# Performance work log

Hardware: AMD Instinct MI355X
Metric: run time of the kernel (lower is better)

## Reference

```python
import jax, jax.numpy as jnp
import numpy as np

B = 65536        # batch of (Z, N) token pairs
V = 512          # vocab size per input
D = 1024         # hidden_dim == embedding_dim
IN = 2 * D       # input_dim = embedding_dim * len(vocab_size)
E = 4            # num_experts (hardcoded in MoEModel)
OUT = 128        # output_dim


def setup_inputs() -> dict:
    key = jax.random.key(0)
    ks = jax.random.split(key, 6)
    x = jax.random.randint(ks[0], (B, 2), 0, V, dtype=jnp.int64)
    emb0 = jax.random.normal(ks[1], (V, D), dtype=jnp.float32)
    emb1 = jax.random.normal(ks[2], (V, D), dtype=jnp.float32)
    W1 = jax.random.normal(ks[3], (E, IN, D), dtype=jnp.float32) * 0.02
    b1 = jnp.zeros((E, D), dtype=jnp.float32)
    W2 = jax.random.normal(ks[4], (E, D, OUT), dtype=jnp.float32) * 0.02
    b2 = jnp.zeros((E, OUT), dtype=jnp.float32)
    Wg = jax.random.normal(ks[5], (IN, E), dtype=jnp.float32) * 0.02
    bg = jnp.zeros((E,), dtype=jnp.float32)
    return {"x": x, "emb0": emb0, "emb1": emb1, "W1": W1, "b1": b1,
            "W2": W2, "b2": b2, "Wg": Wg, "bg": bg}


def reference(x, emb0, emb1, W1, b1, W2, b2, Wg, bg):
    # embed_input: gather each column's embedding and concat -> [B, IN]
    e = jnp.concatenate([emb0[x[:, 0]], emb1[x[:, 1]]], axis=1)
    # gating network: softmax(MuReadout(e)) -> [B, E]
    gates = jax.nn.softmax(e @ Wg + bg, axis=-1)
    # all 4 experts run densely: Linear -> SiLU -> MuReadout, batched over E
    h = jax.nn.silu(jnp.einsum('bi,eid->bed', e, W1) + b1)      # [B, E, D]
    expert_out = jnp.einsum('bed,edo->beo', h, W2) + b2          # [B, E, OUT]
    # einsum('ij,ikj->ik') combine: softmax-weighted mixture over experts
    out = jnp.einsum('be,beo->bo', gates, expert_out)            # [B, OUT]
    return out
```

## Files before the change

kernel.cpp:

```cpp
#include <hip/hip_runtime.h>


typedef __attribute__((ext_vector_type(8))) short short8;
typedef __attribute__((ext_vector_type(4))) float f32x4;

static __device__ __forceinline__ unsigned short f2b(float f) {
  unsigned int u = __builtin_bit_cast(unsigned int, f);
  u += 0x7fffu + ((u >> 16) & 1u);
  return (unsigned short)(u >> 16);
}
static __device__ __forceinline__ float bflo(unsigned int u) {
  return __builtin_bit_cast(float, u << 16);
}
static __device__ __forceinline__ float bfhi(unsigned int u) {
  return __builtin_bit_cast(float, u & 0xffff0000u);
}

#define BARRIER() do { asm volatile("s_waitcnt lgkmcnt(0)" ::: "memory"); \
                       __builtin_amdgcn_s_barrier(); } while (0)

__global__ void prep_g(const float* __restrict__ emb0, const float* __restrict__ emb1,
                       const float* __restrict__ Wg, const float* __restrict__ bg,
                       float* __restrict__ G0, float* __restrict__ G1) {
  const int bid = blockIdx.x;
  const int half = bid >> 9;
  const int v = bid & 511;
  const float* __restrict__ emb = half ? emb1 : emb0;
  const float* __restrict__ wg = Wg + (size_t)half * 1024 * 4;
  float a0 = 0.f, a1 = 0.f, a2 = 0.f, a3 = 0.f;
  for (int i = threadIdx.x; i < 1024; i += 256) {
    const float ev = emb[(size_t)v * 1024 + i];
    const float4 w = *(const float4*)(wg + (size_t)i * 4);
    a0 += ev * w.x; a1 += ev * w.y; a2 += ev * w.z; a3 += ev * w.w;
  }
  __shared__ float red[4][256];
  red[0][threadIdx.x] = a0; red[1][threadIdx.x] = a1;
  red[2][threadIdx.x] = a2; red[3][threadIdx.x] = a3;
  __syncthreads();
  for (int s = 128; s > 0; s >>= 1) {
    if (threadIdx.x < s) {
      red[0][threadIdx.x] += red[0][threadIdx.x + s];
      red[1][threadIdx.x] += red[1][threadIdx.x + s];
      red[2][threadIdx.x] += red[2][threadIdx.x + s];
      red[3][threadIdx.x] += red[3][threadIdx.x + s];
    }
    __syncthreads();
  }
  if (threadIdx.x < 4) {
    const float val = red[threadIdx.x][0] + (half == 0 ? bg[threadIdx.x] : 0.f);
    (half ? G1 : G0)[(size_t)v * 4 + threadIdx.x] = val;
  }
}

__global__ void prep_w2(const float* __restrict__ W2, unsigned short* __restrict__ W2T) {
  __shared__ float st[64][65];
  const int kt = blockIdx.x, ot = blockIdx.y;
  const int tid = threadIdx.x;
  for (int it = 0; it < 16; ++it) {
    const int idx = it * 256 + tid;
    const int k = idx >> 6, o = idx & 63;
    st[k][o] = W2[(size_t)(kt * 64 + k) * 128 + ot * 64 + o];
  }
  __syncthreads();
  for (int it = 0; it < 4; ++it) {
    const int idx = it * 256 + tid;
    const int o = idx >> 4, c = idx & 15;
    const unsigned int p0 =
        (unsigned int)f2b(st[c * 4 + 0][o]) | ((unsigned int)f2b(st[c * 4 + 1][o]) << 16);
    const unsigned int p1 =
        (unsigned int)f2b(st[c * 4 + 2][o]) | ((unsigned int)f2b(st[c * 4 + 3][o]) << 16);
    *(uint2*)(W2T + (size_t)(ot * 64 + o) * 4096 + kt * 64 + c * 4) = make_uint2(p0, p1);
  }
}

__global__ void prep_emb(const float* __restrict__ emb0, const float* __restrict__ emb1,
                         unsigned short* __restrict__ E0, unsigned short* __restrict__ E1) {
  const float* __restrict__ src = blockIdx.y ? emb1 : emb0;
  unsigned short* __restrict__ dst = blockIdx.y ? E1 : E0;
  const size_t base = (size_t)blockIdx.x * 2048 + (size_t)threadIdx.x * 8;
  const float4 lo = *(const float4*)(src + base);
  const float4 hi = *(const float4*)(src + base + 4);
  short8 o;
  o[0] = (short)f2b(lo.x); o[1] = (short)f2b(lo.y);
  o[2] = (short)f2b(lo.z); o[3] = (short)f2b(lo.w);
  o[4] = (short)f2b(hi.x); o[5] = (short)f2b(hi.y);
  o[6] = (short)f2b(hi.z); o[7] = (short)f2b(hi.w);
  *(short8*)(dst + base) = o;
}

__global__ void prep_w1t(const float* __restrict__ W1, unsigned short* __restrict__ W1T) {
  __shared__ float st[64][65];
  const int z = blockIdx.y;
  const int kt = blockIdx.x >> 4, dt = blockIdx.x & 15;
  const int e = z >> 1, half = z & 1;
  const int tid = threadIdx.x;
  const int r = tid >> 2, cg = (tid & 3) * 16;
  const float* src = W1 + ((size_t)e * 2048 + half * 1024 + kt * 64 + r) * 1024 + dt * 64 + cg;
#pragma unroll
  for (int j = 0; j < 4; ++j) {
    const float4 v = *(const float4*)(src + j * 4);
    st[r][cg + j * 4 + 0] = v.x; st[r][cg + j * 4 + 1] = v.y;
    st[r][cg + j * 4 + 2] = v.z; st[r][cg + j * 4 + 3] = v.w;
  }
  __syncthreads();
  const int dr = tid >> 2, kb = (tid & 3) * 16;
  short8 o0, o1;
#pragma unroll
  for (int m = 0; m < 8; ++m) o0[m] = (short)f2b(st[kb + m][dr]);
#pragma unroll
  for (int m = 0; m < 8; ++m) o1[m] = (short)f2b(st[kb + 8 + m][dr]);
  unsigned short* dst = W1T + ((size_t)z * 1024 + dt * 64 + dr) * 1024 + kt * 64 + kb;
  *(short8*)dst = o0;
  *(short8*)(dst + 8) = o1;
}

__launch_bounds__(256, 2)
__global__ void build_tables(const unsigned short* __restrict__ E0,
                             const unsigned short* __restrict__ E1,
                             const unsigned short* __restrict__ W1T,
                             const float* __restrict__ b1,
                             unsigned short* __restrict__ T0, unsigned short* __restrict__ T1) {
  __shared__ unsigned short At[128 * 64];
  __shared__ unsigned short Bt[64 * 64];

  const int bid = blockIdx.x;
  const int z = bid >> 6, rem = bid & 63;
  const int vt = rem >> 4, dt = rem & 15;
  const int e = z >> 1, half = z & 1;
  const unsigned short* __restrict__ E = half ? E1 : E0;
  const unsigned short* __restrict__ Wp = W1T + (size_t)z * 1024 * 1024;
  unsigned short* __restrict__ Tout = (half ? T1 : T0) + (size_t)e * 512 * 1024;

  const int tid = threadIdx.x, lane = tid & 63, wave = tid >> 6;
  const int wm = wave >> 1, wn = wave & 1;

  const int arow = tid >> 1, ah = tid & 1;
  int wAoff[4];
#pragma unroll
  for (int i = 0; i < 4; ++i)
    wAoff[i] = arow * 128 + ((ah * 64 + i * 16) ^ ((arow & 7) << 4));
  const int bcol = tid >> 2, bc = tid & 3;
  int wBoff[2];
#pragma unroll
  for (int i = 0; i < 2; ++i)
    wBoff[i] = bcol * 128 + ((bc * 32 + i * 16) ^ ((bcol & 7) << 4));

  const unsigned short* aSrc = E + (size_t)(vt * 128 + arow) * 1024 + ah * 32;
  const unsigned short* bSrc = Wp + (size_t)(dt * 64 + bcol) * 1024 + bc * 16;

  const int kq = (lane >> 4) * 16;
  int rAoff[4], rAsw[4], rBoff[2], rBsw[2];
#pragma unroll
  for (int mi = 0; mi < 4; ++mi) {
    const int ra = wm * 64 + mi * 16 + (lane & 15);
    rAoff[mi] = ra * 128; rAsw[mi] = (ra & 7) << 4;
  }
#pragma unroll
  for (int ni = 0; ni < 2; ++ni) {
    const int cb = wn * 32 + ni * 16 + (lane & 15);
    rBoff[ni] = cb * 128; rBsw[ni] = (cb & 7) << 4;
  }

  f32x4 acc[4][2] = {};
  uint4 ea[4]; uint4 eb[2];

  auto issueLoads = [&](int kt2) {
    const int k0 = kt2 * 64;
#pragma unroll
    for (int i = 0; i < 4; ++i) ea[i] = *(const uint4*)(aSrc + k0 + i * 8);
#pragma unroll
    for (int i = 0; i < 2; ++i) eb[i] = *(const uint4*)(bSrc + k0 + i * 8);
  };

  issueLoads(0);
  for (int kt2 = 0; kt2 < 16; ++kt2) {
    BARRIER();
#pragma unroll
    for (int i = 0; i < 4; ++i) *(uint4*)((char*)At + wAoff[i]) = ea[i];
#pragma unroll
    for (int i = 0; i < 2; ++i) *(uint4*)((char*)Bt + wBoff[i]) = eb[i];
    if (kt2 < 15) issueLoads(kt2 + 1);
    BARRIER();
#pragma unroll
    for (int kk = 0; kk < 2; ++kk) {
      const int kb = kk * 64 + kq;
      short8 af[4], bfr[2];
#pragma unroll
      for (int mi = 0; mi < 4; ++mi)
        af[mi] = *(const short8*)((char*)At + rAoff[mi] + (kb ^ rAsw[mi]));
#pragma unroll
      for (int ni = 0; ni < 2; ++ni)
        bfr[ni] = *(const short8*)((char*)Bt + rBoff[ni] + (kb ^ rBsw[ni]));
#pragma unroll
      for (int mi = 0; mi < 4; ++mi)
#pragma unroll
        for (int ni = 0; ni < 2; ++ni)
          acc[mi][ni] = __builtin_amdgcn_mfma_f32_16x16x32_bf16(af[mi], bfr[ni], acc[mi][ni], 0, 0, 0);
    }
  }
  const float* bb = b1 + (size_t)e * 1024;
#pragma unroll
  for (int ni = 0; ni < 2; ++ni) {
    const int dcol = dt * 64 + wn * 32 + ni * 16 + (lane & 15);
    const float bias = (half == 0) ? bb[dcol] : 0.f;
#pragma unroll
    for (int mi = 0; mi < 4; ++mi) {
      const int vrow0 = vt * 128 + wm * 64 + mi * 16 + ((lane >> 4) << 2);
      const f32x4 a = acc[mi][ni];
#pragma unroll
      for (int j = 0; j < 4; ++j)
        Tout[(size_t)(vrow0 + j) * 1024 + dcol] = f2b(a[j] + bias);
    }
  }
}

__launch_bounds__(512, 4)
__global__ void moe_main(const int* __restrict__ X,
                         const unsigned short* __restrict__ T0,
                         const unsigned short* __restrict__ T1,
                         const unsigned short* __restrict__ W2T,
                         const float* __restrict__ G0,
                         const float* __restrict__ G1,
                         const float* __restrict__ b2v,
                         float* __restrict__ out) {
  __shared__ unsigned short At[128 * 64];
  __shared__ unsigned short Bt[128 * 64];
  __shared__ float gl[128 * 4];
  __shared__ int xs0[128], xs1[128];

  const int tid = threadIdx.x, lane = tid & 63, wave = tid >> 6;
  const int wm = wave >> 1, wn = wave & 1;
  int bid = blockIdx.x;
  bid = (bid & 7) * 64 + (bid >> 3);
  const int b0 = bid * 128;

  if (tid < 128) {
    const int b = b0 + tid;
    const int x0 = X[2 * b], x1 = X[2 * b + 1];
    xs0[tid] = x0; xs1[tid] = x1;
    const float4 l0 = *(const float4*)(G0 + 4 * x0);
    const float4 l1 = *(const float4*)(G1 + 4 * x1);
    const float z0 = l0.x + l1.x, z1 = l0.y + l1.y;
    const float z2 = l0.z + l1.z, z3 = l0.w + l1.w;
    const float m = fmaxf(fmaxf(z0, z1), fmaxf(z2, z3));
    const float e0 = __expf(z0 - m), e1 = __expf(z1 - m);
    const float e2 = __expf(z2 - m), e3 = __expf(z3 - m);
    const float inv = __builtin_amdgcn_rcpf(e0 + e1 + e2 + e3);
    *(float4*)(&gl[4 * tid]) = make_float4(e0 * inv, e1 * inv, e2 * inv, e3 * inv);
  }
  __syncthreads();

  const int arow = tid >> 2, ac = tid & 3;
  const int sx0 = xs0[arow], sx1 = xs1[arow];
  const float4 grow = *(const float4*)(&gl[4 * arow]);
  int wOff[2];
#pragma unroll
  for (int i = 0; i < 2; ++i)
    wOff[i] = arow * 128 + ((ac * 32 + i * 16) ^ ((arow & 7) << 4));

  const int kq = (lane >> 4) * 16;
  int rAoff[2], rAsw[2], rBoff[4], rBsw[4];
#pragma unroll
  for (int mi = 0; mi < 2; ++mi) {
    const int ra = wm * 32 + mi * 16 + (lane & 15);
    rAoff[mi] = ra * 128; rAsw[mi] = (ra & 7) << 4;
  }
#pragma unroll
  for (int ni = 0; ni < 4; ++ni) {
    const int cb = wn * 64 + ni * 16 + (lane & 15);
    rBoff[ni] = cb * 128; rBsw[ni] = (cb & 7) << 4;
  }

  f32x4 acc[2][4] = {};
  uint4 ua[2], ub[2], bw[2];

  auto issueLoads = [&](int t) {
    const int e = t >> 4, d0 = (t & 15) << 6;
    const unsigned short* p0 = T0 + (((size_t)(e * 512 + sx0)) << 10) + d0 + ac * 16;
    const unsigned short* p1 = T1 + (((size_t)(e * 512 + sx1)) << 10) + d0 + ac * 16;
    const unsigned short* pb = W2T + (size_t)arow * 4096 + t * 64 + ac * 16;
    ua[0] = *(const uint4*)p0; ua[1] = *(const uint4*)(p0 + 8);
    ub[0] = *(const uint4*)p1; ub[1] = *(const uint4*)(p1 + 8);
    bw[0] = *(const uint4*)pb; bw[1] = *(const uint4*)(pb + 8);
  };

  issueLoads(0);
  for (int t = 0; t < 64; ++t) {
    const int e = t >> 4;
    const float g = (e == 0) ? grow.x : (e == 1) ? grow.y : (e == 2) ? grow.z : grow.w;
    short8 sa[2];
#pragma unroll
    for (int i = 0; i < 2; ++i) {
      float f[8];
      f[0] = bflo(ua[i].x) + bflo(ub[i].x);
      f[1] = bfhi(ua[i].x) + bfhi(ub[i].x);
      f[2] = bflo(ua[i].y) + bflo(ub[i].y);
      f[3] = bfhi(ua[i].y) + bfhi(ub[i].y);
      f[4] = bflo(ua[i].z) + bflo(ub[i].z);
      f[5] = bfhi(ua[i].z) + bfhi(ub[i].z);
      f[6] = bflo(ua[i].w) + bflo(ub[i].w);
      f[7] = bfhi(ua[i].w) + bfhi(ub[i].w);
      short8 o8;
#pragma unroll
      for (int j = 0; j < 8; ++j) {
        const float tv = f[j];
        const float sg = g * tv * __builtin_amdgcn_rcpf(1.f + __expf(-tv));
        o8[j] = (short)f2b(sg);
      }
      sa[i] = o8;
    }
    BARRIER();
    *(uint4*)((char*)At + wOff[0]) = *(uint4*)&sa[0];
    *(uint4*)((char*)At + wOff[1]) = *(uint4*)&sa[1];
    *(uint4*)((char*)Bt + wOff[0]) = bw[0];
    *(uint4*)((char*)Bt + wOff[1]) = bw[1];
    if (t < 63) issueLoads(t + 1);
    BARRIER();
#pragma unroll
    for (int kk = 0; kk < 2; ++kk) {
      const int kb = kk * 64 + kq;
      short8 af[2], bfr[4];
#pragma unroll
      for (int mi = 0; mi < 2; ++mi)
        af[mi] = *(const short8*)((char*)At + rAoff[mi] + (kb ^ rAsw[mi]));
#pragma unroll
      for (int ni = 0; ni < 4; ++ni)
        bfr[ni] = *(const short8*)((char*)Bt + rBoff[ni] + (kb ^ rBsw[ni]));
#pragma unroll
      for (int mi = 0; mi < 2; ++mi)
#pragma unroll
        for (int ni = 0; ni < 4; ++ni)
          acc[mi][ni] = __builtin_amdgcn_mfma_f32_16x16x32_bf16(af[mi], bfr[ni], acc[mi][ni], 0, 0, 0);
    }
  }

#pragma unroll
  for (int ni = 0; ni < 4; ++ni) {
    const int col = wn * 64 + ni * 16 + (lane & 15);
    const float c0 = b2v[col], c1 = b2v[128 + col];
    const float c2 = b2v[256 + col], c3 = b2v[384 + col];
#pragma unroll
    for (int mi = 0; mi < 2; ++mi) {
      const int row0 = wm * 32 + mi * 16 + ((lane >> 4) << 2);
      const f32x4 a = acc[mi][ni];
#pragma unroll
      for (int j = 0; j < 4; ++j) {
        const int row = row0 + j;
        const float4 g = *(const float4*)(&gl[4 * row]);
        out[(size_t)(b0 + row) * 128 + col] = a[j] + g.x * c0 + g.y * c1 + g.z * c2 + g.w * c3;
      }
    }
  }
}

extern "C" void kernel_launch(void* const* d_in, const int* in_sizes, int n_in,
                              void* d_out, int out_size, void* d_ws, size_t ws_size,
                              hipStream_t stream) {
  const int*   X    = (const int*)  d_in[0];
  const float* emb0 = (const float*)d_in[1];
  const float* emb1 = (const float*)d_in[2];
  const float* W1   = (const float*)d_in[3];
  const float* b1   = (const float*)d_in[4];
  const float* W2   = (const float*)d_in[5];
  const float* b2   = (const float*)d_in[6];
  const float* Wg   = (const float*)d_in[7];
  const float* bg   = (const float*)d_in[8];
  float* out = (float*)d_out;

  char* ws = (char*)d_ws;
  const size_t MB = 1024 * 1024;
  unsigned short* T0  = (unsigned short*)(ws);
  unsigned short* T1  = (unsigned short*)(ws + 4 * MB);
  unsigned short* W2T = (unsigned short*)(ws + 8 * MB);
  float* G0 = (float*)(ws + 9 * MB);
  float* G1 = (float*)(ws + 9 * MB + 8192);
  unsigned short* E0  = (unsigned short*)(ws + 10 * MB);
  unsigned short* E1  = (unsigned short*)(ws + 11 * MB);
  unsigned short* W1T = (unsigned short*)(ws + 12 * MB);

  hipLaunchKernelGGL(prep_emb, dim3(256, 2), dim3(256), 0, stream, emb0, emb1, E0, E1);
  hipLaunchKernelGGL(prep_w1t, dim3(256, 8), dim3(256), 0, stream, W1, W1T);
  hipLaunchKernelGGL(prep_w2, dim3(64, 2), dim3(256), 0, stream, W2, W2T);
  hipLaunchKernelGGL(prep_g, dim3(1024), dim3(256), 0, stream, emb0, emb1, Wg, bg, G0, G1);
  hipLaunchKernelGGL(build_tables, dim3(512), dim3(256), 0, stream, E0, E1, W1T, b1, T0, T1);
  hipLaunchKernelGGL(moe_main, dim3(512), dim3(512), 0, stream, X, T0, T1, W2T, G0, G1, b2, out);
}
```

Baseline: 346.0 us.

## Fuse prep kernels, double-buffer register prefetch, and stage output stores through LDS

Merges the four preprocessing kernels into a single launch dispatched by block index, and switches bf16 packing to the hardware v_cvt_pk_bf16_f32 instruction. build_tables drops to 64x64 tiles with twice as many blocks and higher occupancy, double-buffers its register prefetch, and writes results through LDS so global stores are coalesced. moe_main double-buffers the gathered table loads, raises wave priority around the MFMA section, and stages the fp32 output through LDS for vectorized coalesced stores. These changes target launch overhead, load latency and scattered stores, at the cost of more registers and extra barriers.

Result: slower. 387.5 us (+12.0%).

```diff
diff --git a/kernel.cpp b/kernel.cpp
--- a/kernel.cpp
+++ b/kernel.cpp
@@ -15,116 +15,119 @@
 static __device__ __forceinline__ float bfhi(unsigned int u) {
   return __builtin_bit_cast(float, u & 0xffff0000u);
 }
+static __device__ __forceinline__ unsigned int cvtpk(float a, float b) {
+  unsigned int r;
+  asm("v_cvt_pk_bf16_f32 %0, %1, %2" : "=v"(r) : "v"(a), "v"(b));
+  return r;
+}
 
 #define BARRIER() do { asm volatile("s_waitcnt lgkmcnt(0)" ::: "memory"); \
                        __builtin_amdgcn_s_barrier(); } while (0)
 
-__global__ void prep_g(const float* __restrict__ emb0, const float* __restrict__ emb1,
-                       const float* __restrict__ Wg, const float* __restrict__ bg,
-                       float* __restrict__ G0, float* __restrict__ G1) {
+__global__ void prep_all(const float* __restrict__ emb0, const float* __restrict__ emb1,
+                         const float* __restrict__ Wg, const float* __restrict__ bg,
+                         const float* __restrict__ W2, const float* __restrict__ W1,
+                         float* __restrict__ G0, float* __restrict__ G1,
+                         unsigned short* __restrict__ E0, unsigned short* __restrict__ E1,
+                         unsigned short* __restrict__ W2T, unsigned short* __restrict__ W1T) {
+  __shared__ __align__(16) char sm[16640];
   const int bid = blockIdx.x;
-  const int half = bid >> 9;
-  const int v = bid & 511;
-  const float* __restrict__ emb = half ? emb1 : emb0;
-  const float* __restrict__ wg = Wg + (size_t)half * 1024 * 4;
-  float a0 = 0.f, a1 = 0.f, a2 = 0.f, a3 = 0.f;
-  for (int i = threadIdx.x; i < 1024; i += 256) {
-    const float ev = emb[(size_t)v * 1024 + i];
-    const float4 w = *(const float4*)(wg + (size_t)i * 4);
-    a0 += ev * w.x; a1 += ev * w.y; a2 += ev * w.z; a3 += ev * w.w;
-  }
-  __shared__ float red[4][256];
-  red[0][threadIdx.x] = a0; red[1][threadIdx.x] = a1;
-  red[2][threadIdx.x] = a2; red[3][threadIdx.x] = a3;
-  __syncthreads();
-  for (int s = 128; s > 0; s >>= 1) {
-    if (threadIdx.x < s) {
-      red[0][threadIdx.x] += red[0][threadIdx.x + s];
-      red[1][threadIdx.x] += red[1][threadIdx.x + s];
-      red[2][threadIdx.x] += red[2][threadIdx.x + s];
-      red[3][threadIdx.x] += red[3][threadIdx.x + s];
-    }
+  const int tid = threadIdx.x;
+  if (bid < 1024) {
+    float (*red)[256] = (float(*)[256])sm;
+    const int half = bid >> 9, v = bid & 511;
+    const float* __restrict__ emb = half ? emb1 : emb0;
+    const float* __restrict__ wg = Wg + (size_t)half * 1024 * 4;
+    float a0 = 0.f, a1 = 0.f, a2 = 0.f, a3 = 0.f;
+    for (int i = tid; i < 1024; i += 256) {
+      const float ev = emb[(size_t)v * 1024 + i];
+      const float4 w = *(const float4*)(wg + (size_t)i * 4);
+      a0 += ev * w.x; a1 += ev * w.y; a2 += ev * w.z; a3 += ev * w.w;
+    }
+    red[0][tid] = a0; red[1][tid] = a1; red[2][tid] = a2; red[3][tid] = a3;
     __syncthreads();
-  }
-  if (threadIdx.x < 4) {
-    const float val = red[threadIdx.x][0] + (half == 0 ? bg[threadIdx.x] : 0.f);
-    (half ? G1 : G0)[(size_t)v * 4 + threadIdx.x] = val;
-  }
-}
-
-__global__ void prep_w2(const float* __restrict__ W2, unsigned short* __restrict__ W2T) {
-  __shared__ float st[64][65];
-  const int kt = blockIdx.x, ot = blockIdx.y;
-  const int tid = threadIdx.x;
-  for (int it = 0; it < 16; ++it) {
-    const int idx = it * 256 + tid;
-    const int k = idx >> 6, o = idx & 63;
-    st[k][o] = W2[(size_t)(kt * 64 + k) * 128 + ot * 64 + o];
-  }
-  __syncthreads();
-  for (int it = 0; it < 4; ++it) {
-    const int idx = it * 256 + tid;
-    const int o = idx >> 4, c = idx & 15;
-    const unsigned int p0 =
-        (unsigned int)f2b(st[c * 4 + 0][o]) | ((unsigned int)f2b(st[c * 4 + 1][o]) << 16);
-    const unsigned int p1 =
-        (unsigned int)f2b(st[c * 4 + 2][o]) | ((unsigned int)f2b(st[c * 4 + 3][o]) << 16);
-    *(uint2*)(W2T + (size_t)(ot * 64 + o) * 4096 + kt * 64 + c * 4) = make_uint2(p0, p1);
-  }
-}
-
-__global__ void prep_emb(const float* __restrict__ emb0, const float* __restrict__ emb1,
-                         unsigned short* __restrict__ E0, unsigned short* __restrict__ E1) {
-  const float* __restrict__ src = blockIdx.y ? emb1 : emb0;
-  unsigned short* __restrict__ dst = blockIdx.y ? E1 : E0;
-  const size_t base = (size_t)blockIdx.x * 2048 + (size_t)threadIdx.x * 8;
-  const float4 lo = *(const float4*)(src + base);
-  const float4 hi = *(const float4*)(src + base + 4);
-  short8 o;
-  o[0] = (short)f2b(lo.x); o[1] = (short)f2b(lo.y);
-  o[2] = (short)f2b(lo.z); o[3] = (short)f2b(lo.w);
-  o[4] = (short)f2b(hi.x); o[5] = (short)f2b(hi.y);
-  o[6] = (short)f2b(hi.z); o[7] = (short)f2b(hi.w);
-  *(short8*)(dst + base) = o;
-}
-
-__global__ void prep_w1t(const float* __restrict__ W1, unsigned short* __restrict__ W1T) {
-  __shared__ float st[64][65];
-  const int z = blockIdx.y;
-  const int kt = blockIdx.x >> 4, dt = blockIdx.x & 15;
-  const int e = z >> 1, half = z & 1;
-  const int tid = threadIdx.x;
-  const int r = tid >> 2, cg = (tid & 3) * 16;
-  const float* src = W1 + ((size_t)e * 2048 + half * 1024 + kt * 64 + r) * 1024 + dt * 64 + cg;
-#pragma unroll
-  for (int j = 0; j < 4; ++j) {
-    const float4 v = *(const float4*)(src + j * 4);
-    st[r][cg + j * 4 + 0] = v.x; st[r][cg + j * 4 + 1] = v.y;
-    st[r][cg + j * 4 + 2] = v.z; st[r][cg + j * 4 + 3] = v.w;
-  }
-  __syncthreads();
-  const int dr = tid >> 2, kb = (tid & 3) * 16;
-  short8 o0, o1;
-#pragma unroll
-  for (int m = 0; m < 8; ++m) o0[m] = (short)f2b(st[kb + m][dr]);
-#pragma unroll
-  for (int m = 0; m < 8; ++m) o1[m] = (short)f2b(st[kb + 8 + m][dr]);
-  unsigned short* dst = W1T + ((size_t)z * 1024 + dt * 64 + dr) * 1024 + kt * 64 + kb;
-  *(short8*)dst = o0;
-  *(short8*)(dst + 8) = o1;
-}
-
-__launch_bounds__(256, 2)
+    for (int s = 128; s > 0; s >>= 1) {
+      if (tid < s) {
+        red[0][tid] += red[0][tid + s]; red[1][tid] += red[1][tid + s];
+        red[2][tid] += red[2][tid + s]; red[3][tid] += red[3][tid + s];
+      }
+      __syncthreads();
+    }
+    if (tid < 4) {
+      const float val = red[tid][0] + (half == 0 ? bg[tid] : 0.f);
+      (half ? G1 : G0)[(size_t)v * 4 + tid] = val;
+    }
+  } else if (bid < 1536) {
+    const int idx = bid - 1024;
+    const int half = idx >> 8, blk = idx & 255;
+    const float* __restrict__ src = half ? emb1 : emb0;
+    unsigned short* __restrict__ dst = half ? E1 : E0;
+    const size_t base = (size_t)blk * 2048 + (size_t)tid * 8;
+    const float4 lo = *(const float4*)(src + base);
+    const float4 hi = *(const float4*)(src + base + 4);
+    uint4 o;
+    o.x = cvtpk(lo.x, lo.y); o.y = cvtpk(lo.z, lo.w);
+    o.z = cvtpk(hi.x, hi.y); o.w = cvtpk(hi.z, hi.w);
+    *(uint4*)(dst + base) = o;
+  } else if (bid < 1664) {
+    float (*st)[65] = (float(*)[65])sm;
+    const int idx = bid - 1536;
+    const int kt = idx & 63, ot = idx >> 6;
+    for (int it = 0; it < 16; ++it) {
+      const int i2 = it * 256 + tid;
+      const int k = i2 >> 6, o = i2 & 63;
+      st[k][o] = W2[(size_t)(kt * 64 + k) * 128 + ot * 64 + o];
+    }
+    __syncthreads();
+    for (int it = 0; it < 4; ++it) {
+      const int i2 = it * 256 + tid;
+      const int o = i2 >> 4, c = i2 & 15;
+      const unsigned int p0 = cvtpk(st[c * 4 + 0][o], st[c * 4 + 1][o]);
+      const unsigned int p1 = cvtpk(st[c * 4 + 2][o], st[c * 4 + 3][o]);
+      *(uint2*)(W2T + (size_t)(ot * 64 + o) * 4096 + kt * 64 + c * 4) = make_uint2(p0, p1);
+    }
+  } else {
+    float (*st)[65] = (float(*)[65])sm;
+    const int idx = bid - 1664;
+    const int z = idx >> 8, xx = idx & 255;
+    const int kt = xx >> 4, dt = xx & 15;
+    const int e = z >> 1, half = z & 1;
+    const int r = tid >> 2, cg = (tid & 3) * 16;
+    const float* src = W1 + ((size_t)e * 2048 + half * 1024 + kt * 64 + r) * 1024 + dt * 64 + cg;
+#pragma unroll
+    for (int j = 0; j < 4; ++j) {
+      const float4 v = *(const float4*)(src + j * 4);
+      st[r][cg + j * 4 + 0] = v.x; st[r][cg + j * 4 + 1] = v.y;
+      st[r][cg + j * 4 + 2] = v.z; st[r][cg + j * 4 + 3] = v.w;
+    }
+    __syncthreads();
+    const int dr = tid >> 2, kb = (tid & 3) * 16;
+    uint4 o0, o1;
+    o0.x = cvtpk(st[kb + 0][dr], st[kb + 1][dr]);
+    o0.y = cvtpk(st[kb + 2][dr], st[kb + 3][dr]);
+    o0.z = cvtpk(st[kb + 4][dr], st[kb + 5][dr]);
+    o0.w = cvtpk(st[kb + 6][dr], st[kb + 7][dr]);
+    o1.x = cvtpk(st[kb + 8][dr], st[kb + 9][dr]);
+    o1.y = cvtpk(st[kb + 10][dr], st[kb + 11][dr]);
+    o1.z = cvtpk(st[kb + 12][dr], st[kb + 13][dr]);
+    o1.w = cvtpk(st[kb + 14][dr], st[kb + 15][dr]);
+    unsigned short* dst = W1T + ((size_t)z * 1024 + dt * 64 + dr) * 1024 + kt * 64 + kb;
+    *(uint4*)dst = o0;
+    *(uint4*)(dst + 8) = o1;
+  }
+}
+
+__launch_bounds__(256, 4)
 __global__ void build_tables(const unsigned short* __restrict__ E0,
                              const unsigned short* __restrict__ E1,
                              const unsigned short* __restrict__ W1T,
                              const float* __restrict__ b1,
                              unsigned short* __restrict__ T0, unsigned short* __restrict__ T1) {
-  __shared__ unsigned short At[128 * 64];
-  __shared__ unsigned short Bt[64 * 64];
+  __shared__ __align__(16) unsigned short At[64 * 64];
+  __shared__ __align__(16) unsigned short Bt[64 * 64];
 
   const int bid = blockIdx.x;
-  const int z = bid >> 6, rem = bid & 63;
+  const int z = bid >> 7, rem = bid & 127;
   const int vt = rem >> 4, dt = rem & 15;
   const int e = z >> 1, half = z & 1;
   const unsigned short* __restrict__ E = half ? E1 : E0;
@@ -134,83 +137,101 @@
   const int tid = threadIdx.x, lane = tid & 63, wave = tid >> 6;
   const int wm = wave >> 1, wn = wave & 1;
 
-  const int arow = tid >> 1, ah = tid & 1;
-  int wAoff[4];
-#pragma unroll
-  for (int i = 0; i < 4; ++i)
-    wAoff[i] = arow * 128 + ((ah * 64 + i * 16) ^ ((arow & 7) << 4));
-  const int bcol = tid >> 2, bc = tid & 3;
-  int wBoff[2];
+  const int arow = tid >> 2, ac = tid & 3;
+  int wOff[2];
 #pragma unroll
   for (int i = 0; i < 2; ++i)
-    wBoff[i] = bcol * 128 + ((bc * 32 + i * 16) ^ ((bcol & 7) << 4));
-
-  const unsigned short* aSrc = E + (size_t)(vt * 128 + arow) * 1024 + ah * 32;
-  const unsigned short* bSrc = Wp + (size_t)(dt * 64 + bcol) * 1024 + bc * 16;
+    wOff[i] = arow * 128 + ((ac * 32 + i * 16) ^ ((arow & 7) << 4));
+  const unsigned short* aSrc = E + (size_t)(vt * 64 + arow) * 1024 + ac * 16;
+  const unsigned short* bSrc = Wp + (size_t)(dt * 64 + arow) * 1024 + ac * 16;
 
   const int kq = (lane >> 4) * 16;
-  int rAoff[4], rAsw[4], rBoff[2], rBsw[2];
-#pragma unroll
-  for (int mi = 0; mi < 4; ++mi) {
-    const int ra = wm * 64 + mi * 16 + (lane & 15);
+  int rAoff[2], rAsw[2], rBoff[2], rBsw[2];
+#pragma unroll
+  for (int mi = 0; mi < 2; ++mi) {
+    const int ra = wm * 32 + mi * 16 + (lane & 15);
     rAoff[mi] = ra * 128; rAsw[mi] = (ra & 7) << 4;
-  }
-#pragma unroll
-  for (int ni = 0; ni < 2; ++ni) {
-    const int cb = wn * 32 + ni * 16 + (lane & 15);
-    rBoff[ni] = cb * 128; rBsw[ni] = (cb & 7) << 4;
-  }
-
-  f32x4 acc[4][2] = {};
-  uint4 ea[4]; uint4 eb[2];
-
-  auto issueLoads = [&](int kt2) {
-    const int k0 = kt2 * 64;
-#pragma unroll
-    for (int i = 0; i < 4; ++i) ea[i] = *(const uint4*)(aSrc + k0 + i * 8);
-#pragma unroll
-    for (int i = 0; i < 2; ++i) eb[i] = *(const uint4*)(bSrc + k0 + i * 8);
-  };
-
-  issueLoads(0);
-  for (int kt2 = 0; kt2 < 16; ++kt2) {
-    BARRIER();
-#pragma unroll
-    for (int i = 0; i < 4; ++i) *(uint4*)((char*)At + wAoff[i]) = ea[i];
-#pragma unroll
-    for (int i = 0; i < 2; ++i) *(uint4*)((char*)Bt + wBoff[i]) = eb[i];
-    if (kt2 < 15) issueLoads(kt2 + 1);
-    BARRIER();
+    const int cb = wn * 32 + mi * 16 + (lane & 15);
+    rBoff[mi] = cb * 128; rBsw[mi] = (cb & 7) << 4;
+  }
+
+  f32x4 acc[2][2] = {};
+  uint4 eaA[2], ebA[2], eaB[2], ebB[2];
+
+  auto issue = [&](int kt, uint4* ea, uint4* eb) {
+    const int k0 = kt * 64;
+    ea[0] = *(const uint4*)(aSrc + k0); ea[1] = *(const uint4*)(aSrc + k0 + 8);
+    eb[0] = *(const uint4*)(bSrc + k0); eb[1] = *(const uint4*)(bSrc + k0 + 8);
+  };
+  auto mfmaStep = [&]() {
 #pragma unroll
     for (int kk = 0; kk < 2; ++kk) {
       const int kb = kk * 64 + kq;
-      short8 af[4], bfr[2];
-#pragma unroll
-      for (int mi = 0; mi < 4; ++mi)
+      short8 af[2], bfr[2];
+#pragma unroll
+      for (int mi = 0; mi < 2; ++mi)
         af[mi] = *(const short8*)((char*)At + rAoff[mi] + (kb ^ rAsw[mi]));
 #pragma unroll
       for (int ni = 0; ni < 2; ++ni)
         bfr[ni] = *(const short8*)((char*)Bt + rBoff[ni] + (kb ^ rBsw[ni]));
 #pragma unroll
-      for (int mi = 0; mi < 4; ++mi)
+      for (int mi = 0; mi < 2; ++mi)
 #pragma unroll
         for (int ni = 0; ni < 2; ++ni)
           acc[mi][ni] = __builtin_amdgcn_mfma_f32_16x16x32_bf16(af[mi], bfr[ni], acc[mi][ni], 0, 0, 0);
     }
-  }
+  };
+
+  issue(0, eaA, ebA);
+  issue(1, eaB, ebB);
+  for (int kt = 0; kt < 16; kt += 2) {
+    BARRIER();
+#pragma unroll
+    for (int i = 0; i < 2; ++i) {
+      *(uint4*)((char*)At + wOff[i]) = eaA[i];
+      *(uint4*)((char*)Bt + wOff[i]) = ebA[i];
+    }
+    if (kt + 2 < 16) issue(kt + 2, eaA, ebA);
+    BARRIER();
+    __builtin_amdgcn_s_setprio(1);
+    mfmaStep();
+    __builtin_amdgcn_s_setprio(0);
+    BARRIER();
+#pragma unroll
+    for (int i = 0; i < 2; ++i) {
+      *(uint4*)((char*)At + wOff[i]) = eaB[i];
+      *(uint4*)((char*)Bt + wOff[i]) = ebB[i];
+    }
+    if (kt + 3 < 16) issue(kt + 3, eaB, ebB);
+    BARRIER();
+    __builtin_amdgcn_s_setprio(1);
+    mfmaStep();
+    __builtin_amdgcn_s_setprio(0);
+  }
+
   const float* bb = b1 + (size_t)e * 1024;
+  unsigned short* fs = At;
+  BARRIER();
 #pragma unroll
   for (int ni = 0; ni < 2; ++ni) {
-    const int dcol = dt * 64 + wn * 32 + ni * 16 + (lane & 15);
-    const float bias = (half == 0) ? bb[dcol] : 0.f;
-#pragma unroll
-    for (int mi = 0; mi < 4; ++mi) {
-      const int vrow0 = vt * 128 + wm * 64 + mi * 16 + ((lane >> 4) << 2);
+    const int lc = wn * 32 + ni * 16 + (lane & 15);
+    const float bias = (half == 0) ? bb[dt * 64 + lc] : 0.f;
+#pragma unroll
+    for (int mi = 0; mi < 2; ++mi) {
+      const int r0 = wm * 32 + mi * 16 + ((lane >> 4) << 2);
       const f32x4 a = acc[mi][ni];
 #pragma unroll
-      for (int j = 0; j < 4; ++j)
-        Tout[(size_t)(vrow0 + j) * 1024 + dcol] = f2b(a[j] + bias);
-    }
+      for (int j = 0; j < 4; ++j) fs[(r0 + j) * 64 + lc] = f2b(a[j] + bias);
+    }
+  }
+  BARRIER();
+  {
+    const int r = tid >> 2, c = (tid & 3) * 16;
+    const uint4 w0 = *(const uint4*)(fs + r * 64 + c);
+    const uint4 w1 = *(const uint4*)(fs + r * 64 + c + 8);
+    unsigned short* op = Tout + (size_t)(vt * 64 + r) * 1024 + dt * 64 + c;
+    *(uint4*)op = w0;
+    *(uint4*)(op + 8) = w1;
   }
 }
 
@@ -223,10 +244,12 @@
                          const float* __restrict__ G1,
                          const float* __restrict__ b2v,
                          float* __restrict__ out) {
-  __shared__ unsigned short At[128 * 64];
-  __shared__ unsigned short Bt[128 * 64];
-  __shared__ float gl[128 * 4];
-  __shared__ int xs0[128], xs1[128];
+  __shared__ __align__(16) char smem[35840];
+  unsigned short* At = (unsigned short*)smem;
+  unsigned short* Bt = (unsigned short*)(smem + 16384);
+  float* gl = (float*)(smem + 32768);
+  int* xs0 = (int*)(smem + 34816);
+  int* xs1 = (int*)(smem + 35328);
 
   const int tid = threadIdx.x, lane = tid & 63, wave = tid >> 6;
   const int wm = wave >> 1, wn = wave & 1;
@@ -272,50 +295,37 @@
   }
 
   f32x4 acc[2][4] = {};
-  uint4 ua[2], ub[2], bw[2];
-
-  auto issueLoads = [&](int t) {
+  uint4 uaA[2], ubA[2], uaB[2], ubB[2], bw[2];
+
+  auto issueA = [&](int t, uint4* ua, uint4* ub) {
     const int e = t >> 4, d0 = (t & 15) << 6;
     const unsigned short* p0 = T0 + (((size_t)(e * 512 + sx0)) << 10) + d0 + ac * 16;
     const unsigned short* p1 = T1 + (((size_t)(e * 512 + sx1)) << 10) + d0 + ac * 16;
-    const unsigned short* pb = W2T + (size_t)arow * 4096 + t * 64 + ac * 16;
     ua[0] = *(const uint4*)p0; ua[1] = *(const uint4*)(p0 + 8);
     ub[0] = *(const uint4*)p1; ub[1] = *(const uint4*)(p1 + 8);
+  };
+  auto issueB = [&](int t) {
+    const unsigned short* pb = W2T + (size_t)arow * 4096 + t * 64 + ac * 16;
     bw[0] = *(const uint4*)pb; bw[1] = *(const uint4*)(pb + 8);
   };
-
-  issueLoads(0);
-  for (int t = 0; t < 64; ++t) {
-    const int e = t >> 4;
-    const float g = (e == 0) ? grow.x : (e == 1) ? grow.y : (e == 2) ? grow.z : grow.w;
-    short8 sa[2];
+  auto siluPack = [&](const uint4* ua, const uint4* ub, float g, uint4* sw) {
 #pragma unroll
     for (int i = 0; i < 2; ++i) {
-      float f[8];
-      f[0] = bflo(ua[i].x) + bflo(ub[i].x);
-      f[1] = bfhi(ua[i].x) + bfhi(ub[i].x);
-      f[2] = bflo(ua[i].y) + bflo(ub[i].y);
-      f[3] = bfhi(ua[i].y) + bfhi(ub[i].y);
-      f[4] = bflo(ua[i].z) + bflo(ub[i].z);
-      f[5] = bfhi(ua[i].z) + bfhi(ub[i].z);
-      f[6] = bflo(ua[i].w) + bflo(ub[i].w);
-      f[7] = bfhi(ua[i].w) + bfhi(ub[i].w);
-      short8 o8;
-#pragma unroll
-      for (int j = 0; j < 8; ++j) {
-        const float tv = f[j];
-        const float sg = g * tv * __builtin_amdgcn_rcpf(1.f + __expf(-tv));
-        o8[j] = (short)f2b(sg);
+      const unsigned int uu[4] = {ua[i].x, ua[i].y, ua[i].z, ua[i].w};
+      const unsigned int vv[4] = {ub[i].x, ub[i].y, ub[i].z, ub[i].w};
+      unsigned int w[4];
+#pragma unroll
+      for (int p = 0; p < 4; ++p) {
+        const float f0 = bflo(uu[p]) + bflo(vv[p]);
+        const float f1 = bfhi(uu[p]) + bfhi(vv[p]);
+        const float s0 = g * f0 * __builtin_amdgcn_rcpf(1.f + __expf(-f0));
+        const float s1 = g * f1 * __builtin_amdgcn_rcpf(1.f + __expf(-f1));
+        w[p] = cvtpk(s0, s1);
       }
-      sa[i] = o8;
-    }
-    BARRIER();
-    *(uint4*)((char*)At + wOff[0]) = *(uint4*)&sa[0];
-    *(uint4*)((char*)At + wOff[1]) = *(uint4*)&sa[1];
-    *(uint4*)((char*)Bt + wOff[0]) = bw[0];
-    *(uint4*)((char*)Bt + wOff[1]) = bw[1];
-    if (t < 63) issueLoads(t + 1);
-    BARRIER();
+      sw[i] = uint4{w[0], w[1], w[2], w[3]};
+    }
+  };
+  auto mfmaStep = [&]() {
 #pragma unroll
     for (int kk = 0; kk < 2; ++kk) {
       const int kb = kk * 64 + kq;
@@ -331,6 +341,46 @@
 #pragma unroll
         for (int ni = 0; ni < 4; ++ni)
           acc[mi][ni] = __builtin_amdgcn_mfma_f32_16x16x32_bf16(af[mi], bfr[ni], acc[mi][ni], 0, 0, 0);
+    }
+  };
+  auto gsel = [&](int t) -> float {
+    const int e = t >> 4;
+    return (e == 0) ? grow.x : (e == 1) ? grow.y : (e == 2) ? grow.z : grow.w;
+  };
+
+  issueA(0, uaA, ubA);
+  issueB(0);
+  issueA(1, uaB, ubB);
+
+  for (int t = 0; t < 64; t += 2) {
+    {
+      uint4 sw[2];
+      siluPack(uaA, ubA, gsel(t), sw);
+      BARRIER();
+      *(uint4*)((char*)At + wOff[0]) = sw[0];
+      *(uint4*)((char*)At + wOff[1]) = sw[1];
+      *(uint4*)((char*)Bt + wOff[0]) = bw[0];
+      *(uint4*)((char*)Bt + wOff[1]) = bw[1];
+      if (t + 2 < 64) issueA(t + 2, uaA, ubA);
+      issueB(t + 1);
+      BARRIER();
+      __builtin_amdgcn_s_setprio(1);
+      mfmaStep();
+      __builtin_amdgcn_s_setprio(0);
+    }
+    {
+      uint4 sw[2];
+      siluPack(uaB, ubB, gsel(t + 1), sw);
+      BARRIER();
+      *(uint4*)((char*)At + wOff[0]) = sw[0];
+      *(uint4*)((char*)At + wOff[1]) = sw[1];
+      *(uint4*)((char*)Bt + wOff[0]) = bw[0];
+      *(uint4*)((char*)Bt + wOff[1]) = bw[1];
+      if (t + 3 < 64) { issueA(t + 3, uaB, ubB); issueB(t + 2); }
+      BARRIER();
+      __builtin_amdgcn_s_setprio(1);
+      mfmaStep();
+      __builtin_amdgcn_s_setprio(0);
     }
   }
 
@@ -341,15 +391,43 @@
     const float c2 = b2v[256 + col], c3 = b2v[384 + col];
 #pragma unroll
     for (int mi = 0; mi < 2; ++mi) {
-      const int row0 = wm * 32 + mi * 16 + ((lane >> 4) << 2);
-      const f32x4 a = acc[mi][ni];
 #pragma unroll
       for (int j = 0; j < 4; ++j) {
-        const int row = row0 + j;
+        const int row = wm * 32 + mi * 16 + ((lane >> 4) << 2) + j;
         const float4 g = *(const float4*)(&gl[4 * row]);
-        out[(size_t)(b0 + row) * 128 + col] = a[j] + g.x * c0 + g.y * c1 + g.z * c2 + g.w * c3;
+        acc[mi][ni][j] += g.x * c0 + g.y * c1 + g.z * c2 + g.w * c3;
       }
     }
+  }
+  float* fs = (float*)smem;
+#pragma unroll
+  for (int p = 0; p < 2; ++p) {
+    BARRIER();
+    if ((wm >> 1) == p) {
+      const int rbase = (wm & 1) * 32;
+#pragma unroll
+      for (int ni = 0; ni < 4; ++ni) {
+        const int col = wn * 64 + ni * 16 + (lane & 15);
+#pragma unroll
+        for (int mi = 0; mi < 2; ++mi) {
+          const int r0 = rbase + mi * 16 + ((lane >> 4) << 2);
+          const f32x4 a = acc[mi][ni];
+#pragma unroll
+          for (int j = 0; j < 4; ++j) fs[(r0 + j) * 128 + col] = a[j];
+        }
+      }
+    }
+    BARRIER();
+    const int r = tid >> 3, c0 = (tid & 7) * 16;
+    const float4 v0 = *(const float4*)(fs + r * 128 + c0);
+    const float4 v1 = *(const float4*)(fs + r * 128 + c0 + 4);
+    const float4 v2 = *(const float4*)(fs + r * 128 + c0 + 8);
+    const float4 v3 = *(const float4*)(fs + r * 128 + c0 + 12);
+    float* op = out + (size_t)(b0 + p * 64 + r) * 128 + c0;
+    *(float4*)op = v0;
+    *(float4*)(op + 4) = v1;
+    *(float4*)(op + 8) = v2;
+    *(float4*)(op + 12) = v3;
   }
 }
 
@@ -378,10 +456,8 @@
   unsigned short* E1  = (unsigned short*)(ws + 11 * MB);
   unsigned short* W1T = (unsigned short*)(ws + 12 * MB);
 
-  hipLaunchKernelGGL(prep_emb, dim3(256, 2), dim3(256), 0, stream, emb0, emb1, E0, E1);
-  hipLaunchKernelGGL(prep_w1t, dim3(256, 8), dim3(256), 0, stream, W1, W1T);
-  hipLaunchKernelGGL(prep_w2, dim3(64, 2), dim3(256), 0, stream, W2, W2T);
-  hipLaunchKernelGGL(prep_g, dim3(1024), dim3(256), 0, stream, emb0, emb1, Wg, bg, G0, G1);
-  hipLaunchKernelGGL(build_tables, dim3(512), dim3(256), 0, stream, E0, E1, W1T, b1, T0, T1);
+  hipLaunchKernelGGL(prep_all, dim3(3712), dim3(256), 0, stream,
+                     emb0, emb1, Wg, bg, W2, W1, G0, G1, E0, E1, W2T, W1T);
+  hipLaunchKernelGGL(build_tables, dim3(1024), dim3(256), 0, stream, E0, E1, W1T, b1, T0, T1);
   hipLaunchKernelGGL(moe_main, dim3(512), dim3(512), 0, stream, X, T0, T1, W2T, G0, G1, b2, out);
 }
```
